# Optimization experiments

Hardware: AMD Instinct MI355X
Metric: run time of the kernel (lower is better)

Reference implementation:

```python
import jax, jax.numpy as jnp
import numpy as np

DIM, H, W, DEPTH = 256, 64, 64, 4
D_STATE, DT_RANK, D_CONV = 8, 16, 4
G, AGENTS = 8, 4

PKEYS = ['ln_w','ln_b','in_proj_w','conv_w','conv_b','x_proj_w','dt_proj_w','dt_proj_b',
         'A_log','A_b_log','D','out_proj_w','mn_w','mn_b']


def layernorm(x, w, b, eps=1e-5):
    mu = jnp.mean(x, -1, keepdims=True)
    var = jnp.var(x, -1, keepdims=True)
    return (x - mu) * jax.lax.rsqrt(var + eps) * w + b


def causal_conv1d(x, w, b):
    # x: (g, d, L); w: (d, k) depthwise causal conv (pad left k-1)
    k = w.shape[-1]
    xp = jnp.pad(x, ((0, 0), (0, 0), (k - 1, 0)))
    y = jax.lax.conv_general_dilated(xp, w[:, None, :], (1,), 'VALID',
                                     dimension_numbers=('NCH', 'OIH', 'NCH'),
                                     feature_group_count=w.shape[0])
    return y + b[None, :, None]


def selective_scan(u, delta, A, B, C, Dp, z):
    # u, delta, z: (g, d, L); B, C: (g, n, L); A: (d, n); Dp: (d,)
    dT = jnp.moveaxis(delta, -1, 0)
    BT = jnp.moveaxis(B, -1, 0)
    CT = jnp.moveaxis(C, -1, 0)
    uT = jnp.moveaxis(u, -1, 0)
    h0 = jnp.zeros(u.shape[:2] + (A.shape[-1],), u.dtype)  # (g, d, n)

    def step(h, inp):
        d_t, B_t, C_t, u_t = inp  # (g,d),(g,n),(g,n),(g,d)
        h = jnp.exp(d_t[..., None] * A) * h + (d_t * u_t)[..., None] * B_t[:, None, :]
        return h, jnp.einsum('gdn,gn->gd', h, C_t)

    _, ys = jax.lax.scan(step, h0, (dT, BT, CT, uT))
    y = jnp.moveaxis(ys, 0, -1) + Dp[None, :, None] * u
    return y * jax.nn.silu(z)


def ssm_dir(xdl, zdl, p, A):
    # one scan direction of mamba_inner_fn_no_out_proj; xdl, zdl: (g, d, L)
    xc = jax.nn.silu(causal_conv1d(xdl, p['conv_w'], p['conv_b']))
    x_dbl = jnp.einsum('gdl,ed->gel', xc, p['x_proj_w'])  # e = dt_rank + 2n
    dt, B, C = jnp.split(x_dbl, [DT_RANK, DT_RANK + D_STATE], axis=1)
    delta = jax.nn.softplus(jnp.einsum('grl,dr->gdl', dt, p['dt_proj_w'])
                            + p['dt_proj_b'][None, :, None])
    return selective_scan(xc, delta, A, B, C, p['D'], zdl)


def single_mamba_block(x, p):
    # x: (g, L, c)  -- LayerNorm + bidirectional Mamba (bimamba v1) + residual
    skip = x
    xn = layernorm(x, p['ln_w'], p['ln_b'])
    xz = jnp.einsum('glc,ec->gle', xn, p['in_proj_w'])  # (g, L, 2d), no bias
    xx, z = jnp.split(xz, 2, axis=-1)
    xdl = jnp.swapaxes(xx, 1, 2)
    zdl = jnp.swapaxes(z, 1, 2)
    y_f = ssm_dir(xdl, zdl, p, -jnp.exp(p['A_log']))
    y_b = jnp.flip(ssm_dir(jnp.flip(xdl, -1), jnp.flip(zdl, -1), p, -jnp.exp(p['A_b_log'])), -1)
    y = 0.5 * (y_f + y_b)  # if_devide_out=True
    out = jnp.einsum('gdl,od->glo', y, p['out_proj_w'])  # no bias
    out = layernorm(out, p['mn_w'], p['mn_b'])  # use_norm=True
    return out + skip


def _forward(data, plist, record_len):
    b, c, h, w = data.shape
    rl = np.asarray(record_len)
    seg = jnp.asarray(np.repeat(np.arange(rl.shape[0]), rl))
    means = jax.ops.segment_sum(data, seg, num_segments=rl.shape[0]) \
        / jnp.asarray(rl, data.dtype)[:, None, None, None]
    x = means.reshape(rl.shape[0], c, h * w).transpose(0, 2, 1)  # (G, L, C)
    for i in range(DEPTH):
        p = {k: v[i] for k, v in zip(PKEYS, plist)}
        x = single_mamba_block(x, p)
    return x.transpose(0, 2, 1).reshape(rl.shape[0], c, h, w)


def setup_inputs() -> dict:
    key = jax.random.key(0)
    ks = jax.random.split(key, 8)
    nrm = lambda k, shape, sc: jax.random.normal(k, shape, jnp.float32) * sc
    Alog = jnp.zeros((DEPTH, DIM, D_STATE), jnp.float32) \
        + jnp.log(jnp.arange(1, D_STATE + 1, dtype=jnp.float32))
    return {
        'data': jax.random.normal(ks[0], (G * AGENTS, DIM, H, W), jnp.float32),
        'ln_w': jnp.ones((DEPTH, DIM)), 'ln_b': jnp.zeros((DEPTH, DIM)),
        'in_proj_w': nrm(ks[1], (DEPTH, 2 * DIM, DIM), 0.02),
        'conv_w': nrm(ks[2], (DEPTH, DIM, D_CONV), 0.3),
        'conv_b': jnp.zeros((DEPTH, DIM)),
        'x_proj_w': nrm(ks[3], (DEPTH, DT_RANK + 2 * D_STATE, DIM), 0.02),
        'dt_proj_w': nrm(ks[4], (DEPTH, DIM, DT_RANK), 0.1),
        'dt_proj_b': jnp.full((DEPTH, DIM), float(np.log(np.expm1(0.01))), jnp.float32),
        'A_log': Alog, 'A_b_log': Alog,
        'D': jnp.ones((DEPTH, DIM)),
        'out_proj_w': nrm(ks[5], (DEPTH, DIM, DIM), 0.02),
        'mn_w': jnp.ones((DEPTH, DIM)), 'mn_b': jnp.zeros((DEPTH, DIM)),
        'record_len': jnp.full((G,), AGENTS, dtype=jnp.int32),
    }


def reference(data, ln_w, ln_b, in_proj_w, conv_w, conv_b, x_proj_w, dt_proj_w, dt_proj_b,
              A_log, A_b_log, D, out_proj_w, mn_w, mn_b, record_len):
    plist = [ln_w, ln_b, in_proj_w, conv_w, conv_b, x_proj_w, dt_proj_w, dt_proj_b,
             A_log, A_b_log, D, out_proj_w, mn_w, mn_b]
    return _forward(data, plist, record_len)
```

## Files before the change

### kernel.cpp

```cpp
#include <hip/hip_runtime.h>
#include <hip/hip_bf16.h>
#include <cstdint>
#include <cstddef>

typedef unsigned short u16;
typedef unsigned int   u32;

typedef short s16x8 __attribute__((ext_vector_type(8)));
typedef float f32x4 __attribute__((ext_vector_type(4)));

__device__ __forceinline__ float b2f(u16 u){ u32 x = ((u32)u)<<16; float f; __builtin_memcpy(&f,&x,4); return f; }
__device__ __forceinline__ u16  f2b(float f){ u32 x; __builtin_memcpy(&x,&f,4); u32 r = x + 0x7FFFu + ((x>>16)&1u); return (u16)(r>>16); }

__device__ __forceinline__ void unpack8(uint4 v, float* o){
  o[0]=b2f((u16)v.x); o[1]=b2f((u16)(v.x>>16));
  o[2]=b2f((u16)v.y); o[3]=b2f((u16)(v.y>>16));
  o[4]=b2f((u16)v.z); o[5]=b2f((u16)(v.z>>16));
  o[6]=b2f((u16)v.w); o[7]=b2f((u16)(v.w>>16));
}

__device__ __forceinline__ void gl_lds16(const u16* g, u16* l){
  __builtin_amdgcn_global_load_lds((const __attribute__((address_space(1))) u32*)g,
                                   (__attribute__((address_space(3))) u32*)l, 16, 0, 0);
}

__global__ void k_detect(const u16* __restrict__ lnw, int* __restrict__ flag){
  if (threadIdx.x==0 && blockIdx.x==0) *flag = (lnw[0] == 0x3F80) ? 1 : 0;
}

struct CvtTable { const void* src[14]; u16* dst[14]; int n[14]; };
__global__ void k_cvt(CvtTable t, const int* __restrict__ flag){
  int ti = blockIdx.y;
  int n = t.n[ti];
  int isbf = *flag;
  const u16*  sb = (const u16*)t.src[ti];
  const float* sf = (const float*)t.src[ti];
  u16* d = t.dst[ti];
  for (int i = blockIdx.x*256 + threadIdx.x; i < n; i += gridDim.x*256)
    d[i] = isbf ? sb[i] : f2b(sf[i]);
}

__global__ void k_mean(const void* __restrict__ data, const int* __restrict__ rl,
                       float* __restrict__ x, const int* __restrict__ flag){
  __shared__ float tile[32][129];
  int isbf = *flag;
  const u16*  db = (const u16*)data;
  const float* df_ = (const float*)data;
  int g = blockIdx.z, c0 = blockIdx.y*32, l0 = blockIdx.x*128;
  int tid = threadIdx.x;
  int off=0; for(int i=0;i<g;i++) off += rl[i];
  int cnt = rl[g];
  float inv = 1.0f/(float)cnt;
  for(int it=0; it<16; ++it){
    int idx = it*256 + tid;
    int ci = idx>>7, lj = idx&127;
    float acc = 0.f;
    for(int b=0;b<cnt;b++){
      size_t gi = ((size_t)(off+b)*256 + (c0+ci)) * 4096 + (l0+lj);
      acc += isbf ? b2f(db[gi]) : df_[gi];
    }
    tile[ci][lj] = acc*inv;
  }
  __syncthreads();
  for(int it=0; it<16; ++it){
    int idx = it*256 + tid;
    int lj = idx>>5, ci = idx&31;
    x[ ((size_t)g*4096 + (l0+lj))*256 + (c0+ci) ] = tile[ci][lj];
  }
}

__global__ void k_prep(const u16* __restrict__ dtp, const u16* __restrict__ xpw, u16* __restrict__ bcomb){
  int layer = blockIdx.y, row = blockIdx.x, c = threadIdx.x;
  u16 out;
  if (row < 256){
    float acc = 0.f;
    #pragma unroll
    for(int r=0;r<16;r++)
      acc += b2f(dtp[(size_t)layer*4096 + row*16 + r]) * b2f(xpw[(size_t)layer*8192 + r*256 + c]);
    out = f2b(acc);
  } else if (row < 272){
    out = xpw[(size_t)layer*8192 + (16 + row - 256)*256 + c];
  } else {
    out = 0;
  }
  bcomb[((size_t)layer*384 + row)*256 + c] = out;
}

__global__ void k_ln1(const float* __restrict__ x, u16* __restrict__ xn,
                      const u16* __restrict__ w, const u16* __restrict__ b, int layer){
  int wid = threadIdx.x>>6, lane = threadIdx.x&63;
  int row = blockIdx.x*4 + wid;
  const float* xr = x + (size_t)row*256;
  float4 v = *(const float4*)(xr + lane*4);
  float s = v.x+v.y+v.z+v.w;
  float q = v.x*v.x+v.y*v.y+v.z*v.z+v.w*v.w;
  for(int o=32;o;o>>=1){ s += __shfl_xor(s,o); q += __shfl_xor(q,o); }
  float mu = s*(1.f/256.f);
  float var = q*(1.f/256.f) - mu*mu;
  float rs = rsqrtf(var + 1e-5f);
  const u16* wp = w + layer*256 + lane*4;
  const u16* bp = b + layer*256 + lane*4;
  float vv[4] = {v.x,v.y,v.z,v.w};
  u16 o4[4];
  #pragma unroll
  for(int k2=0;k2<4;k2++) o4[k2] = f2b( (vv[k2]-mu)*rs*b2f(wp[k2]) + b2f(bp[k2]) );
  uint2 ov; ov.x = (u32)o4[0] | ((u32)o4[1]<<16); ov.y = (u32)o4[2] | ((u32)o4[3]<<16);
  *(uint2*)(xn + (size_t)row*256 + lane*4) = ov;
}

template<int MODE>
__global__ __launch_bounds__(256)
void k_gemm(const u16* __restrict__ A, const u16* __restrict__ B,
            u16* __restrict__ C0, int ldC,
            const u16* __restrict__ bias, u16* __restrict__ C1){
  __shared__ u16 As[128*64];
  __shared__ u16 Bs[128*64];
  int tid = threadIdx.x, wid = tid>>6, lane = tid&63;
  int m0 = blockIdx.x*128, n0 = blockIdx.y*128;
  f32x4 acc[4][4];
  #pragma unroll
  for(int i=0;i<4;i++)
    #pragma unroll
    for(int j=0;j<4;j++) acc[i][j] = (f32x4){0.f,0.f,0.f,0.f};
  int lrow  = lane>>3;
  int scol  = ((lane&7) ^ lrow) * 8;
  int rm = (wid&1)*64, cn = (wid>>1)*64;
  for(int k0=0;k0<256;k0+=64){
    #pragma unroll
    for(int it=0; it<4; ++it){
      int chunk = wid*4 + it;
      int row = chunk*8 + lrow;
      gl_lds16(A + (size_t)(m0+row)*256 + k0 + scol, As + chunk*512 + lane*8);
      gl_lds16(B + (size_t)(n0+row)*256 + k0 + scol, Bs + chunk*512 + lane*8);
    }
    __syncthreads();
    #pragma unroll
    for(int kk=0;kk<2;kk++){
      s16x8 af[4], bfr[4];
      #pragma unroll
      for(int i=0;i<4;i++){
        int ar = rm + i*16 + (lane&15);
        int ap = (kk*4 + (lane>>4)) ^ (ar&7);
        af[i]  = *(const s16x8*)(As + ar*64 + ap*8);
        int br = cn + i*16 + (lane&15);
        int bp = (kk*4 + (lane>>4)) ^ (br&7);
        bfr[i] = *(const s16x8*)(Bs + br*64 + bp*8);
      }
      #pragma unroll
      for(int i=0;i<4;i++)
        #pragma unroll
        for(int j=0;j<4;j++)
          acc[i][j] = __builtin_amdgcn_mfma_f32_16x16x32_bf16(af[i], bfr[j], acc[i][j], 0,0,0);
    }
    __syncthreads();
  }
  #pragma unroll
  for(int i=0;i<4;i++){
    #pragma unroll
    for(int j=0;j<4;j++){
      int n  = n0 + cn + j*16 + (lane&15);
      int mB = m0 + rm + i*16 + ((lane>>4)<<2);
      #pragma unroll
      for(int r=0;r<4;r++){
        float val = acc[i][j][r];
        int m = mB + r;
        if (MODE==0){
          C0[(size_t)m*ldC + n] = f2b(val);
        } else {
          if (n < 256){
            float v2 = val + b2f(bias[n]);
            float sp = (v2 > 15.f) ? v2 : __logf(1.f + __expf(v2));
            C0[(size_t)m*256 + n] = f2b(sp);
          } else if (n < 272){
            C1[(size_t)m*16 + (n-256)] = f2b(val);
          }
        }
      }
    }
  }
}

__global__ void k_conv(const u16* __restrict__ xz, const u16* __restrict__ cw,
                       const u16* __restrict__ cb, u16* __restrict__ xcf, u16* __restrict__ xcb_, int layer){
  int l = blockIdx.x, g = blockIdx.y, d = threadIdx.x;
  float w[4];
  #pragma unroll
  for(int j=0;j<4;j++) w[j] = b2f(cw[(size_t)layer*1024 + d*4 + j]);
  float bb = b2f(cb[layer*256 + d]);
  float xv[7];
  #pragma unroll
  for(int t=0;t<7;t++){
    int lp = l - 3 + t;
    xv[t] = (lp>=0 && lp<4096) ? b2f(xz[((size_t)g*4096 + lp)*512 + d]) : 0.f;
  }
  float af = bb, ab = bb;
  #pragma unroll
  for(int j=0;j<4;j++){ af += w[j]*xv[j]; ab += w[j]*xv[6-j]; }
  af = af / (1.f + __expf(-af));
  ab = ab / (1.f + __expf(-ab));
  size_t o = ((size_t)g*4096 + l)*256 + d;
  xcf[o]  = f2b(af);
  xcb_[o] = f2b(ab);
}

__global__ __launch_bounds__(256)
void k_scan1(const u16* __restrict__ df, const u16* __restrict__ db,
             const u16* __restrict__ uf, const u16* __restrict__ ub,
             const u16* __restrict__ bcf, const u16* __restrict__ bcb,
             const u16* __restrict__ Alog, const u16* __restrict__ Ablog,
             float* __restrict__ abuf, float* __restrict__ bbuf, int layer){
  int c = blockIdx.x, g = blockIdx.y, dir = blockIdx.z, d = threadIdx.x;
  const u16* dl = dir ? db : df;
  const u16* uu = dir ? ub : uf;
  const u16* bc = dir ? bcb : bcf;
  const u16* Al = dir ? Ablog : Alog;
  float An[8], h[8], ap[8];
  #pragma unroll
  for(int n=0;n<8;n++){
    An[n] = -__expf(b2f(Al[(size_t)layer*2048 + d*8 + n]));
    h[n] = 0.f; ap[n] = 1.f;
  }
  #pragma unroll 4
  for(int t=0;t<64;t++){
    int ts = c*64 + t;
    int tg = dir ? (4095 - ts) : ts;
    size_t rowo = (size_t)g*4096 + tg;
    float dv = b2f(dl[rowo*256 + d]);
    float uv = b2f(uu[rowo*256 + d]);
    uint4 bv = *(const uint4*)(bc + rowo*16);
    float bn[8]; unpack8(bv, bn);
    float du = dv*uv;
    #pragma unroll
    for(int n=0;n<8;n++){
      float da = __expf(dv*An[n]);
      h[n] = fmaf(da, h[n], du*bn[n]);
      ap[n] *= da;
    }
  }
  size_t base = ((((size_t)dir*8+g)*64 + c)*256 + d)*8;
  *(float4*)(abuf+base)   = (float4){ap[0],ap[1],ap[2],ap[3]};
  *(float4*)(abuf+base+4) = (float4){ap[4],ap[5],ap[6],ap[7]};
  *(float4*)(bbuf+base)   = (float4){h[0],h[1],h[2],h[3]};
  *(float4*)(bbuf+base+4) = (float4){h[4],h[5],h[6],h[7]};
}

__global__ void k_scan2(const float* __restrict__ abuf, const float* __restrict__ bbuf,
                        float* __restrict__ hs){
  int dblk = blockIdx.x, g = blockIdx.y, dir = blockIdx.z;
  int n = threadIdx.x & 7, dd = threadIdx.x >> 3;
  int d = dblk*32 + dd;
  float h = 0.f;
  size_t gofs = (((size_t)dir*8+g)*64);
  for(int c=0;c<64;c++){
    size_t idx = ((gofs + c)*256 + d)*8 + n;
    hs[idx] = h;
    h = fmaf(abuf[idx], h, bbuf[idx]);
  }
}

__global__ __launch_bounds__(256)
void k_scan3(const u16* __restrict__ df, const u16* __restrict__ db,
             const u16* __restrict__ uf, const u16* __restrict__ ub,
             const u16* __restrict__ bcf, const u16* __restrict__ bcb,
             const u16* __restrict__ Alog, const u16* __restrict__ Ablog,
             const u16* __restrict__ Dp, const u16* __restrict__ xz,
             const float* __restrict__ hs,
             u16* __restrict__ yf, u16* __restrict__ yb, int layer){
  int c = blockIdx.x, g = blockIdx.y, dir = blockIdx.z, d = threadIdx.x;
  const u16* dl = dir ? db : df;
  const u16* uu = dir ? ub : uf;
  const u16* bc = dir ? bcb : bcf;
  const u16* Al = dir ? Ablog : Alog;
  u16* yo = dir ? yb : yf;
  float An[8], h[8];
  size_t base = ((((size_t)dir*8+g)*64 + c)*256 + d)*8;
  float4 h0 = *(const float4*)(hs+base);
  float4 h1 = *(const float4*)(hs+base+4);
  h[0]=h0.x; h[1]=h0.y; h[2]=h0.z; h[3]=h0.w;
  h[4]=h1.x; h[5]=h1.y; h[6]=h1.z; h[7]=h1.w;
  #pragma unroll
  for(int n=0;n<8;n++) An[n] = -__expf(b2f(Al[(size_t)layer*2048 + d*8 + n]));
  float Dd = b2f(Dp[layer*256 + d]);
  #pragma unroll 2
  for(int t=0;t<64;t++){
    int ts = c*64 + t;
    int tg = dir ? (4095 - ts) : ts;
    size_t rowo = (size_t)g*4096 + tg;
    float dv = b2f(dl[rowo*256 + d]);
    float uv = b2f(uu[rowo*256 + d]);
    uint4 bv = *(const uint4*)(bc + rowo*16);
    uint4 cv = *(const uint4*)(bc + rowo*16 + 8);
    float bn[8], cn_[8];
    unpack8(bv, bn); unpack8(cv, cn_);
    float du = dv*uv;
    float y = 0.f;
    #pragma unroll
    for(int n=0;n<8;n++){
      float da = __expf(dv*An[n]);
      h[n] = fmaf(da, h[n], du*bn[n]);
      y = fmaf(h[n], cn_[n], y);
    }
    y += Dd*uv;
    float zv = b2f(xz[rowo*512 + 256 + d]);
    y *= zv / (1.f + __expf(-zv));
    yo[rowo*256 + d] = f2b(y);
  }
}

__global__ void k_comb(const u16* __restrict__ yf, const u16* __restrict__ yb, u16* __restrict__ yc){
  size_t i = ((size_t)blockIdx.x*256 + threadIdx.x)*8;
  uint4 a = *(const uint4*)(yf+i);
  uint4 b = *(const uint4*)(yb+i);
  float fa[8], fb[8]; unpack8(a,fa); unpack8(b,fb);
  u32 o[4];
  #pragma unroll
  for(int k2=0;k2<4;k2++){
    u16 lo = f2b(0.5f*(fa[2*k2]  +fb[2*k2]));
    u16 hi = f2b(0.5f*(fa[2*k2+1]+fb[2*k2+1]));
    o[k2] = (u32)lo | ((u32)hi<<16);
  }
  *(uint4*)(yc+i) = (uint4){o[0],o[1],o[2],o[3]};
}

__global__ void k_ln2(const u16* __restrict__ ob, float* __restrict__ x,
                      const u16* __restrict__ w, const u16* __restrict__ b, int layer){
  int wid = threadIdx.x>>6, lane = threadIdx.x&63;
  int row = blockIdx.x*4 + wid;
  uint2 iv = *(const uint2*)(ob + (size_t)row*256 + lane*4);
  float v[4] = { b2f((u16)iv.x), b2f((u16)(iv.x>>16)), b2f((u16)iv.y), b2f((u16)(iv.y>>16)) };
  float s = v[0]+v[1]+v[2]+v[3];
  float q = v[0]*v[0]+v[1]*v[1]+v[2]*v[2]+v[3]*v[3];
  for(int o=32;o;o>>=1){ s += __shfl_xor(s,o); q += __shfl_xor(q,o); }
  float mu = s*(1.f/256.f);
  float var = q*(1.f/256.f) - mu*mu;
  float rs = rsqrtf(var+1e-5f);
  float4* xp = (float4*)(x + (size_t)row*256 + lane*4);
  float4 xv = *xp;
  float xa[4] = {xv.x,xv.y,xv.z,xv.w};
  const u16* wp = w + layer*256 + lane*4;
  const u16* bp = b + layer*256 + lane*4;
  float oo[4];
  #pragma unroll
  for(int k2=0;k2<4;k2++) oo[k2] = xa[k2] + (v[k2]-mu)*rs*b2f(wp[k2]) + b2f(bp[k2]);
  *xp = (float4){oo[0],oo[1],oo[2],oo[3]};
}

__global__ void k_tr(const float* __restrict__ x, void* __restrict__ out, const int* __restrict__ flag){
  __shared__ float tile[32][129];
  int isbf = *flag;
  int l0 = blockIdx.x*128, c0 = blockIdx.y*32, g = blockIdx.z;
  int tid = threadIdx.x;
  for(int it=0; it<16; ++it){
    int idx = it*256 + tid;
    int lj = idx>>5, ci = idx&31;
    tile[ci][lj] = x[((size_t)g*4096 + l0+lj)*256 + c0+ci];
  }
  __syncthreads();
  for(int it=0; it<16; ++it){
    int idx = it*256 + tid;
    int lj = idx&127, ci = idx>>7;
    size_t o = ((size_t)g*256 + c0+ci)*4096 + l0+lj;
    float v = tile[ci][lj];
    if (isbf) ((u16*)out)[o] = f2b(v);
    else      ((float*)out)[o] = v;
  }
}

extern "C" void kernel_launch(void* const* d_in, const int* in_sizes, int n_in,
                              void* d_out, int out_size, void* d_ws, size_t ws_size,
                              hipStream_t stream){
  (void)in_sizes; (void)n_in; (void)out_size; (void)ws_size;
  const int* rl = (const int*)d_in[15];

  char* ws = (char*)d_ws;
  float* X    = (float*)(ws);
  u16*  XN    = (u16*)(ws + 33554432);
  u16*  XZ    = (u16*)(ws + 50331648);
  u16*  XCF   = (u16*)(ws + 83886080);
  u16*  XCB   = (u16*)(ws + 100663296);
  u16*  DF    = (u16*)(ws + 117440512);
  u16*  DB    = (u16*)(ws + 134217728);
  u16*  BCF   = (u16*)(ws + 150994944);
  u16*  BCB   = (u16*)(ws + 152043520);
  u16*  BCOMB = (u16*)(ws + 153092096);
  float* ABUF = (float*)(ws + 153878528);
  float* BBUF = (float*)(ws + 162267136);
  u16*  YF    = (u16*)(ws + 153878528);
  float* HS   = (float*)(ws + 170655744);
  u16*  YB    = (u16*)(ws + 179044352);
  u16*  WCVT  = (u16*)(ws + 195821568);
  int*  FLAG  = (int*)(ws + 197918720);
  u16*  YC    = XN;
  u16*  OUTB  = DF;

  u16* W_lnw  = WCVT + 0;
  u16* W_lnb  = WCVT + 1024;
  u16* W_inp  = WCVT + 2048;
  u16* W_cw   = WCVT + 526336;
  u16* W_cb   = WCVT + 530432;
  u16* W_xp   = WCVT + 531456;
  u16* W_dtw  = WCVT + 564224;
  u16* W_dtb  = WCVT + 580608;
  u16* W_Al   = WCVT + 581632;
  u16* W_Abl  = WCVT + 589824;
  u16* W_D    = WCVT + 598016;
  u16* W_outp = WCVT + 599040;
  u16* W_mnw  = WCVT + 861184;
  u16* W_mnb  = WCVT + 862208;

  k_detect<<<1,64,0,stream>>>((const u16*)d_in[1], FLAG);

  CvtTable t;
  const int idxs[14] = {1,2,3,4,5,6,7,8,9,10,11,12,13,14};
  u16* dsts[14] = {W_lnw,W_lnb,W_inp,W_cw,W_cb,W_xp,W_dtw,W_dtb,W_Al,W_Abl,W_D,W_outp,W_mnw,W_mnb};
  const int ns[14] = {1024,1024,524288,4096,1024,32768,16384,1024,8192,8192,1024,262144,1024,1024};
  for(int i=0;i<14;i++){ t.src[i]=d_in[idxs[i]]; t.dst[i]=dsts[i]; t.n[i]=ns[i]; }
  k_cvt<<<dim3(32,14),256,0,stream>>>(t, FLAG);

  k_mean<<<dim3(32,8,8),256,0,stream>>>(d_in[0], rl, X, FLAG);
  k_prep<<<dim3(384,4),256,0,stream>>>(W_dtw, W_xp, BCOMB);

  for(int layer=0; layer<4; ++layer){
    k_ln1<<<8192,256,0,stream>>>(X, XN, W_lnw, W_lnb, layer);
    k_gemm<0><<<dim3(256,4),256,0,stream>>>(XN, W_inp + (size_t)layer*512*256, XZ, 512, nullptr, nullptr);
    k_conv<<<dim3(4096,8),256,0,stream>>>(XZ, W_cw, W_cb, XCF, XCB, layer);
    k_gemm<1><<<dim3(512,3),256,0,stream>>>(XCF, BCOMB + (size_t)layer*384*256, DF, 256, W_dtb + layer*256, BCF);
    k_scan1<<<dim3(64,8,2),256,0,stream>>>(DF,DB,XCF,XCB,BCF,BCB,W_Al,W_Abl,ABUF,BBUF,layer);
    k_scan2<<<dim3(8,8,2),256,0,stream>>>(ABUF,BBUF,HS);
    k_scan3<<<dim3(64,8,2),256,0,stream>>>(DF,DB,XCF,XCB,BCF,BCB,W_Al,W_Abl,W_D,XZ,HS,YF,YB,layer);
    k_comb<<<4096,256,0,stream>>>(YF,YB,YC);
    k_gemm<0><<<dim3(256,2),256,0,stream>>>(YC, W_outp + (size_t)layer*256*256, OUTB, 256, nullptr, nullptr);
    k_ln2<<<8192,256,0,stream>>>(OUTB, X, W_mnw, W_mnb, layer);
  }
  k_tr<<<dim3(32,8,8),256,0,stream>>>(X, d_out, FLAG);
}
```

Baseline: 1.261 ms.

## Fuse direction combine, out-proj GEMM, post-norm residual and next LayerNorm

Replaces the separate combine, output-projection GEMM, post-LayerNorm and next-layer LayerNorm kernels with one MFMA kernel. It averages the forward and backward outputs while staging A tiles, computes the full 256-wide row, then applies the residual LayerNorm and writes both X and the next layer's normalized input. This removes several full-tensor round trips and launches per layer. Separately, the conv kernel now computes four sequence positions per thread to reuse loaded inputs. The fused kernel uses 512 blocks holding 64 accumulators per thread, which may limit occupancy.

```diff
diff --git a/kernel.cpp b/kernel.cpp
--- a/kernel.cpp
+++ b/kernel.cpp
@@ -182,25 +182,28 @@
 
 __global__ void k_conv(const u16* __restrict__ xz, const u16* __restrict__ cw,
                        const u16* __restrict__ cb, u16* __restrict__ xcf, u16* __restrict__ xcb_, int layer){
-  int l = blockIdx.x, g = blockIdx.y, d = threadIdx.x;
+  int l0 = blockIdx.x*4, g = blockIdx.y, d = threadIdx.x;
   float w[4];
   #pragma unroll
   for(int j=0;j<4;j++) w[j] = b2f(cw[(size_t)layer*1024 + d*4 + j]);
   float bb = b2f(cb[layer*256 + d]);
-  float xv[7];
-  #pragma unroll
-  for(int t=0;t<7;t++){
-    int lp = l - 3 + t;
+  float xv[10];
+  #pragma unroll
+  for(int t=0;t<10;t++){
+    int lp = l0 - 3 + t;
     xv[t] = (lp>=0 && lp<4096) ? b2f(xz[((size_t)g*4096 + lp)*512 + d]) : 0.f;
   }
-  float af = bb, ab = bb;
-  #pragma unroll
-  for(int j=0;j<4;j++){ af += w[j]*xv[j]; ab += w[j]*xv[6-j]; }
-  af = af / (1.f + __expf(-af));
-  ab = ab / (1.f + __expf(-ab));
-  size_t o = ((size_t)g*4096 + l)*256 + d;
-  xcf[o]  = f2b(af);
-  xcb_[o] = f2b(ab);
+  #pragma unroll
+  for(int i=0;i<4;i++){
+    float af = bb, ab = bb;
+    #pragma unroll
+    for(int j=0;j<4;j++){ af += w[j]*xv[i+j]; ab += w[j]*xv[i+6-j]; }
+    af = af / (1.f + __expf(-af));
+    ab = ab / (1.f + __expf(-ab));
+    size_t o = ((size_t)g*4096 + (l0+i))*256 + d;
+    xcf[o]  = f2b(af);
+    xcb_[o] = f2b(ab);
+  }
 }
 
 __global__ __launch_bounds__(256)
@@ -307,42 +310,119 @@
   }
 }
 
-__global__ void k_comb(const u16* __restrict__ yf, const u16* __restrict__ yb, u16* __restrict__ yc){
-  size_t i = ((size_t)blockIdx.x*256 + threadIdx.x)*8;
-  uint4 a = *(const uint4*)(yf+i);
-  uint4 b = *(const uint4*)(yb+i);
-  float fa[8], fb[8]; unpack8(a,fa); unpack8(b,fb);
-  u32 o[4];
-  #pragma unroll
-  for(int k2=0;k2<4;k2++){
-    u16 lo = f2b(0.5f*(fa[2*k2]  +fb[2*k2]));
-    u16 hi = f2b(0.5f*(fa[2*k2+1]+fb[2*k2+1]));
-    o[k2] = (u32)lo | ((u32)hi<<16);
-  }
-  *(uint4*)(yc+i) = (uint4){o[0],o[1],o[2],o[3]};
-}
-
-__global__ void k_ln2(const u16* __restrict__ ob, float* __restrict__ x,
-                      const u16* __restrict__ w, const u16* __restrict__ b, int layer){
-  int wid = threadIdx.x>>6, lane = threadIdx.x&63;
-  int row = blockIdx.x*4 + wid;
-  uint2 iv = *(const uint2*)(ob + (size_t)row*256 + lane*4);
-  float v[4] = { b2f((u16)iv.x), b2f((u16)(iv.x>>16)), b2f((u16)iv.y), b2f((u16)(iv.y>>16)) };
-  float s = v[0]+v[1]+v[2]+v[3];
-  float q = v[0]*v[0]+v[1]*v[1]+v[2]*v[2]+v[3]*v[3];
-  for(int o=32;o;o>>=1){ s += __shfl_xor(s,o); q += __shfl_xor(q,o); }
-  float mu = s*(1.f/256.f);
-  float var = q*(1.f/256.f) - mu*mu;
-  float rs = rsqrtf(var+1e-5f);
-  float4* xp = (float4*)(x + (size_t)row*256 + lane*4);
-  float4 xv = *xp;
-  float xa[4] = {xv.x,xv.y,xv.z,xv.w};
-  const u16* wp = w + layer*256 + lane*4;
-  const u16* bp = b + layer*256 + lane*4;
-  float oo[4];
-  #pragma unroll
-  for(int k2=0;k2<4;k2++) oo[k2] = xa[k2] + (v[k2]-mu)*rs*b2f(wp[k2]) + b2f(bp[k2]);
-  *xp = (float4){oo[0],oo[1],oo[2],oo[3]};
+template<int LAST>
+__global__ __launch_bounds__(256)
+void k_outln(const u16* __restrict__ yf, const u16* __restrict__ yb,
+             const u16* __restrict__ Bw,
+             float* __restrict__ X, u16* __restrict__ xn_next,
+             const u16* __restrict__ mnw, const u16* __restrict__ mnb,
+             const u16* __restrict__ lnw_n, const u16* __restrict__ lnb_n){
+  __shared__ u16 As[64*64];
+  __shared__ u16 Bs[256*64];
+  int tid = threadIdx.x, wid = tid>>6, lane = tid&63;
+  int m0 = blockIdx.x*64;
+  f32x4 acc[16];
+  #pragma unroll
+  for(int j=0;j<16;j++) acc[j] = (f32x4){0.f,0.f,0.f,0.f};
+  int lrow = lane>>3;
+  int scol = ((lane&7) ^ lrow) * 8;
+  for(int k0=0;k0<256;k0+=64){
+    #pragma unroll
+    for(int s=0;s<2;s++){
+      int g2 = tid + s*256;
+      int row = g2>>3, p = g2&7;
+      size_t off = (size_t)(m0+row)*256 + k0 + p*8;
+      uint4 a = *(const uint4*)(yf + off);
+      uint4 b = *(const uint4*)(yb + off);
+      float fa[8], fb[8]; unpack8(a,fa); unpack8(b,fb);
+      u32 o[4];
+      #pragma unroll
+      for(int k2=0;k2<4;k2++){
+        u16 lo = f2b(0.5f*(fa[2*k2]  +fb[2*k2]));
+        u16 hi = f2b(0.5f*(fa[2*k2+1]+fb[2*k2+1]));
+        o[k2] = (u32)lo | ((u32)hi<<16);
+      }
+      *(uint4*)(As + row*64 + ((p ^ (row&7))*8)) = (uint4){o[0],o[1],o[2],o[3]};
+    }
+    #pragma unroll
+    for(int it=0; it<8; ++it){
+      int chunk = wid*8 + it;
+      int row = chunk*8 + lrow;
+      gl_lds16(Bw + (size_t)row*256 + k0 + scol, Bs + chunk*512 + lane*8);
+    }
+    __syncthreads();
+    #pragma unroll
+    for(int kk=0;kk<2;kk++){
+      int ar = wid*16 + (lane&15);
+      int ap = (kk*4 + (lane>>4)) ^ (ar&7);
+      s16x8 af = *(const s16x8*)(As + ar*64 + ap*8);
+      #pragma unroll
+      for(int j=0;j<16;j++){
+        int br = j*16 + (lane&15);
+        int bp = (kk*4 + (lane>>4)) ^ (br&7);
+        s16x8 bf = *(const s16x8*)(Bs + br*64 + bp*8);
+        acc[j] = __builtin_amdgcn_mfma_f32_16x16x32_bf16(af, bf, acc[j], 0,0,0);
+      }
+    }
+    __syncthreads();
+  }
+  int quad = lane>>4;
+  float sm[4]={0,0,0,0}, sq[4]={0,0,0,0};
+  #pragma unroll
+  for(int j=0;j<16;j++)
+    #pragma unroll
+    for(int r=0;r<4;r++){ float v=acc[j][r]; sm[r]+=v; sq[r]+=v*v; }
+  #pragma unroll
+  for(int o=1;o<16;o<<=1)
+    #pragma unroll
+    for(int r=0;r<4;r++){ sm[r]+=__shfl_xor(sm[r],o); sq[r]+=__shfl_xor(sq[r],o); }
+  float mu[4], rs[4];
+  #pragma unroll
+  for(int r=0;r<4;r++){
+    mu[r] = sm[r]*(1.f/256.f);
+    float var = sq[r]*(1.f/256.f) - mu[r]*mu[r];
+    rs[r] = rsqrtf(var + 1e-5f);
+  }
+  #pragma unroll
+  for(int j=0;j<16;j++){
+    int col = j*16 + (lane&15);
+    float w = b2f(mnw[col]), bb = b2f(mnb[col]);
+    #pragma unroll
+    for(int r=0;r<4;r++){
+      int m = m0 + wid*16 + quad*4 + r;
+      float xn = X[(size_t)m*256 + col] + (acc[j][r]-mu[r])*rs[r]*w + bb;
+      X[(size_t)m*256 + col] = xn;
+      acc[j][r] = xn;
+    }
+  }
+  if (!LAST){
+    float sm2[4]={0,0,0,0}, sq2[4]={0,0,0,0};
+    #pragma unroll
+    for(int j=0;j<16;j++)
+      #pragma unroll
+      for(int r=0;r<4;r++){ float v=acc[j][r]; sm2[r]+=v; sq2[r]+=v*v; }
+    #pragma unroll
+    for(int o=1;o<16;o<<=1)
+      #pragma unroll
+      for(int r=0;r<4;r++){ sm2[r]+=__shfl_xor(sm2[r],o); sq2[r]+=__shfl_xor(sq2[r],o); }
+    float mu2[4], rs2[4];
+    #pragma unroll
+    for(int r=0;r<4;r++){
+      mu2[r] = sm2[r]*(1.f/256.f);
+      float var = sq2[r]*(1.f/256.f) - mu2[r]*mu2[r];
+      rs2[r] = rsqrtf(var + 1e-5f);
+    }
+    #pragma unroll
+    for(int j=0;j<16;j++){
+      int col = j*16 + (lane&15);
+      float w = b2f(lnw_n[col]), bb = b2f(lnb_n[col]);
+      #pragma unroll
+      for(int r=0;r<4;r++){
+        int m = m0 + wid*16 + quad*4 + r;
+        xn_next[(size_t)m*256 + col] = f2b((acc[j][r]-mu2[r])*rs2[r]*w + bb);
+      }
+    }
+  }
 }
 
 __global__ void k_tr(const float* __restrict__ x, void* __restrict__ out, const int* __restrict__ flag){
@@ -390,8 +470,6 @@
   u16*  YB    = (u16*)(ws + 179044352);
   u16*  WCVT  = (u16*)(ws + 195821568);
   int*  FLAG  = (int*)(ws + 197918720);
-  u16*  YC    = XN;
-  u16*  OUTB  = DF;
 
   u16* W_lnw  = WCVT + 0;
   u16* W_lnb  = WCVT + 1024;
@@ -419,18 +497,24 @@
 
   k_mean<<<dim3(32,8,8),256,0,stream>>>(d_in[0], rl, X, FLAG);
   k_prep<<<dim3(384,4),256,0,stream>>>(W_dtw, W_xp, BCOMB);
+  k_ln1<<<8192,256,0,stream>>>(X, XN, W_lnw, W_lnb, 0);
 
   for(int layer=0; layer<4; ++layer){
-    k_ln1<<<8192,256,0,stream>>>(X, XN, W_lnw, W_lnb, layer);
     k_gemm<0><<<dim3(256,4),256,0,stream>>>(XN, W_inp + (size_t)layer*512*256, XZ, 512, nullptr, nullptr);
-    k_conv<<<dim3(4096,8),256,0,stream>>>(XZ, W_cw, W_cb, XCF, XCB, layer);
+    k_conv<<<dim3(1024,8),256,0,stream>>>(XZ, W_cw, W_cb, XCF, XCB, layer);
     k_gemm<1><<<dim3(512,3),256,0,stream>>>(XCF, BCOMB + (size_t)layer*384*256, DF, 256, W_dtb + layer*256, BCF);
     k_scan1<<<dim3(64,8,2),256,0,stream>>>(DF,DB,XCF,XCB,BCF,BCB,W_Al,W_Abl,ABUF,BBUF,layer);
     k_scan2<<<dim3(8,8,2),256,0,stream>>>(ABUF,BBUF,HS);
     k_scan3<<<dim3(64,8,2),256,0,stream>>>(DF,DB,XCF,XCB,BCF,BCB,W_Al,W_Abl,W_D,XZ,HS,YF,YB,layer);
-    k_comb<<<4096,256,0,stream>>>(YF,YB,YC);
-    k_gemm<0><<<dim3(256,2),256,0,stream>>>(YC, W_outp + (size_t)layer*256*256, OUTB, 256, nullptr, nullptr);
-    k_ln2<<<8192,256,0,stream>>>(OUTB, X, W_mnw, W_mnb, layer);
+    if (layer < 3){
+      k_outln<0><<<512,256,0,stream>>>(YF, YB, W_outp + (size_t)layer*256*256, X, XN,
+                                       W_mnw + layer*256, W_mnb + layer*256,
+                                       W_lnw + (layer+1)*256, W_lnb + (layer+1)*256);
+    } else {
+      k_outln<1><<<512,256,0,stream>>>(YF, YB, W_outp + (size_t)layer*256*256, X, XN,
+                                       W_mnw + layer*256, W_mnb + layer*256,
+                                       W_lnw, W_lnb);
+    }
   }
   k_tr<<<dim3(32,8,8),256,0,stream>>>(X, d_out, FLAG);
 }
```

New measurement: 1.147 ms. 1.1x faster.
